# Kernel tuning notes

Measured on AMD Instinct MI355X. Metric: run time of the kernel, lower is better.

## Reference

```python
import jax, jax.numpy as jnp
import numpy as np

IGNORE_INDEX = -100
BETA = 0.1

B, T, H, V = 4, 512, 1024, 32000  # sequences, tokens/seq, hidden, vocab


def setup_inputs() -> dict:
    key = jax.random.key(0)
    ks = jax.random.split(key, 9)
    scale = 1.0 / np.sqrt(H)
    return {
        "_input": jax.random.normal(ks[0], (B * T, H), jnp.float32),
        "weight": jax.random.normal(ks[1], (V, H), jnp.float32) * scale,
        "target": jax.random.randint(ks[2], (B * T,), 0, V, jnp.int64),
        "bias": jax.random.normal(ks[3], (V,), jnp.float32) * 0.01,
        "preference_labels": jax.random.bernoulli(ks[4], 0.5, (B,)),
        "ref_input": jax.random.normal(ks[5], (B * T, H), jnp.float32),
        "ref_weight": jax.random.normal(ks[6], (V, H), jnp.float32) * scale,
        "ref_bias": jax.random.normal(ks[7], (V,), jnp.float32) * 0.01,
        "kl": jax.random.uniform(ks[8], (1,), jnp.float32),
    }


def _seq_log_prob(x, w, b, target):
    # x: (B*T, H), w: (V, H), b: (V,) -> per-sequence summed target logprob (B,)
    logits = x @ w.T + b  # (B*T, V) -- the tensor the fused kernel avoids
    logp = jax.nn.log_softmax(logits, axis=-1)
    safe_tgt = jnp.clip(target, 0, logp.shape[-1] - 1)
    tok_logp = jnp.take_along_axis(logp, safe_tgt[:, None], axis=-1)[:, 0]
    mask = target != IGNORE_INDEX
    tok_logp = jnp.where(mask, tok_logp, 0.0).reshape(B, T)
    return tok_logp.sum(axis=-1)  # average_log_prob=False


def reference(_input, weight, target, bias, preference_labels, ref_input, ref_weight, ref_bias, kl):
    pol_logp = _seq_log_prob(_input, weight, bias, target)          # (B,)
    ref_logp = _seq_log_prob(ref_input, ref_weight, ref_bias, target)  # (B,)
    logratios = pol_logp - ref_logp
    multiplier = jnp.where(preference_labels, 1.0, -1.0)
    losses = 1.0 - jax.nn.sigmoid(BETA * (logratios - kl[0]) * multiplier)
    loss = losses.sum() / target.shape[0]  # divide by full_target.shape[0] = B*T
    rewards = BETA * logratios
    chosen_rewards_sum = (rewards * preference_labels).sum()
    rejected_rewards_sum = (rewards * (~preference_labels)).sum()
    return loss, chosen_rewards_sum, rejected_rewards_sum
```

## Files before the change

kernel.cpp:

```cpp
#include <hip/hip_runtime.h>

#define BT    2048
#define HDIM  1024
#define VDIM  32000
#define NSEQ  4
#define BETA  0.1f
#define IGNORE_IDX (-100)

typedef __attribute__((ext_vector_type(8))) short bf16x8;
typedef __attribute__((ext_vector_type(8))) unsigned short u16x8;
typedef __attribute__((ext_vector_type(4))) float f32x4;

#define WS_BF_BYTE  32768
#define XBF_OFF     0
#define XRBF_OFF    (BT * HDIM)
#define WBF_OFF     (2 * BT * HDIM)
#define WRBF_OFF    (2 * BT * HDIM + VDIM * HDIM)
#define CVT_TOTAL   (2 * BT * HDIM + 2 * VDIM * HDIM)
#define WS_NEED     ((size_t)WS_BF_BYTE + (size_t)CVT_TOTAL * 2)

__device__ __forceinline__ unsigned short f2bf_rne(float f) {
  unsigned int u = __builtin_bit_cast(unsigned int, f);
  u += 0x7fffu + ((u >> 16) & 1u);
  return (unsigned short)(u >> 16);
}

__device__ __forceinline__ u16x8 cvt8(float4 a, float4 b) {
  u16x8 v;
  v[0] = f2bf_rne(a.x); v[1] = f2bf_rne(a.y); v[2] = f2bf_rne(a.z); v[3] = f2bf_rne(a.w);
  v[4] = f2bf_rne(b.x); v[5] = f2bf_rne(b.y); v[6] = f2bf_rne(b.z); v[7] = f2bf_rne(b.w);
  return v;
}

__global__ __launch_bounds__(256) void kto_zero_ws(float* p) {
  p[blockIdx.x * 256 + threadIdx.x] = 0.0f;
}

__global__ __launch_bounds__(256) void kto_convert(
    const float* __restrict__ X, const float* __restrict__ Xr,
    const float* __restrict__ W, const float* __restrict__ Wr,
    unsigned short* __restrict__ bf)
{
  size_t gid8 = ((size_t)blockIdx.x * 256 + threadIdx.x) * 8;
  if (gid8 >= (size_t)CVT_TOTAL) return;
  const float* src; size_t off;
  if (gid8 < (size_t)XRBF_OFF)      { src = X;  off = gid8; }
  else if (gid8 < (size_t)WBF_OFF)  { src = Xr; off = gid8 - XRBF_OFF; }
  else if (gid8 < (size_t)WRBF_OFF) { src = W;  off = gid8 - WBF_OFF; }
  else                              { src = Wr; off = gid8 - WRBF_OFF; }
  const float4* p = (const float4*)(src + off);
  float4 a = p[0], b = p[1];
  *(u16x8*)(bf + gid8) = cvt8(a, b);
}

#define GLD16(g, l) __builtin_amdgcn_global_load_lds( \
    (const __attribute__((address_space(1))) unsigned int*)(g), \
    (__attribute__((address_space(3))) unsigned int*)(l), 16, 0, 0)

__global__ __launch_bounds__(256) void kto_lse_gemm_fast(
    const unsigned short* __restrict__ bf,
    const float* __restrict__ Bp, const float* __restrict__ Br,
    const int* __restrict__ target,
    float* __restrict__ ws_se, float* __restrict__ ws_tg)
{
  const int model = blockIdx.z;
  const unsigned short* __restrict__ Xb = bf + (model ? XRBF_OFF : XBF_OFF);
  const unsigned short* __restrict__ Wb = bf + (model ? WRBF_OFF : WBF_OFF);
  const float* __restrict__ Bv = model ? Br : Bp;

  __shared__ unsigned short Asm[128 * 32];
  __shared__ unsigned short Bsm[128 * 32];

  const int tid  = threadIdx.x;
  const int wave = tid >> 6;
  const int lane = tid & 63;
  const int q    = lane >> 4;
  const int c    = lane & 15;
  const int mW   = (wave >> 1) * 64;
  const int nW   = (wave & 1) * 64;
  const int mBase = blockIdx.x * 128;
  const int nBase = blockIdx.y * 128;

  const int lrow = lane >> 2;
  const int lchk = (lane & 3) ^ ((lane >> 3) & 3);

  const char* gsrc[4];
  unsigned short* ldst[4];
  #pragma unroll
  for (int j = 0; j < 4; ++j) {
    const int seg = wave * 4 + j;
    if (seg < 8) {
      const int row = mBase + seg * 16 + lrow;
      gsrc[j] = (const char*)Xb + (size_t)row * (HDIM * 2) + lchk * 16;
      ldst[j] = &Asm[seg * 512];
    } else {
      const int row = nBase + (seg - 8) * 16 + lrow;
      gsrc[j] = (const char*)Wb + (size_t)row * (HDIM * 2) + lchk * 16;
      ldst[j] = &Bsm[(seg - 8) * 512];
    }
  }

  const int swz = (q ^ ((c >> 1) & 3)) * 8;

  f32x4 acc[4][4] = {};

  for (int kt = 0; kt < HDIM / 32; ++kt) {
    __syncthreads();
    const size_t kb = (size_t)kt * 64;
    #pragma unroll
    for (int j = 0; j < 4; ++j)
      GLD16(gsrc[j] + kb, ldst[j]);
    __syncthreads();

    bf16x8 afr[4], bfr[4];
    #pragma unroll
    for (int mi = 0; mi < 4; ++mi)
      afr[mi] = *(const bf16x8*)&Asm[(mW + mi * 16 + c) * 32 + swz];
    #pragma unroll
    for (int ni = 0; ni < 4; ++ni)
      bfr[ni] = *(const bf16x8*)&Bsm[(nW + ni * 16 + c) * 32 + swz];
    #pragma unroll
    for (int mi = 0; mi < 4; ++mi)
      #pragma unroll
      for (int ni = 0; ni < 4; ++ni)
        acc[mi][ni] = __builtin_amdgcn_mfma_f32_16x16x32_bf16(afr[mi], bfr[ni], acc[mi][ni], 0, 0, 0);
  }

  float se_acc[4][4] = {};
  float tg_acc[4][4] = {};
  int tgt_idx[4][4];
  #pragma unroll
  for (int mi = 0; mi < 4; ++mi)
    #pragma unroll
    for (int r = 0; r < 4; ++r)
      tgt_idx[mi][r] = target[mBase + mW + mi * 16 + q * 4 + r];

  #pragma unroll
  for (int ni = 0; ni < 4; ++ni) {
    const int col = nBase + nW + ni * 16 + c;
    const float bv = Bv[col];
    #pragma unroll
    for (int mi = 0; mi < 4; ++mi)
      #pragma unroll
      for (int r = 0; r < 4; ++r) {
        float logit = acc[mi][ni][r] + bv;
        se_acc[mi][r] += __expf(logit);
        if (tgt_idx[mi][r] == col) tg_acc[mi][r] += logit;
      }
  }

  #pragma unroll
  for (int mi = 0; mi < 4; ++mi)
    #pragma unroll
    for (int r = 0; r < 4; ++r) {
      float s = se_acc[mi][r];
      float t = tg_acc[mi][r];
      #pragma unroll
      for (int off = 1; off < 16; off <<= 1) {
        s += __shfl_xor(s, off, 64);
        t += __shfl_xor(t, off, 64);
      }
      if (c == ((mi << 2) | r)) {
        const int row = mBase + mW + mi * 16 + q * 4 + r;
        atomicAdd(&ws_se[model * BT + row], s);
        atomicAdd(&ws_tg[model * BT + row], t);
      }
    }
}

#define SBM 128
#define SBN 128
#define SBK 32
#define SVSLICE 1280
#define SNITER  (SVSLICE / SBN)
#define SKTILES (HDIM / SBK)
#define SLDK    (SBK + 8)

__device__ __forceinline__ void cvt_store8s(unsigned short* dst, float4 a, float4 b) {
  *(u16x8*)dst = cvt8(a, b);
}

__global__ __launch_bounds__(256) void kto_lse_gemm_slow(
    const float* __restrict__ Xp, const float* __restrict__ Wp, const float* __restrict__ Bp,
    const float* __restrict__ Xr, const float* __restrict__ Wr, const float* __restrict__ Br,
    const int* __restrict__ target, float* __restrict__ ws_se, float* __restrict__ ws_tg)
{
  const int model = blockIdx.z;
  const float* __restrict__ X  = model ? Xr : Xp;
  const float* __restrict__ W  = model ? Wr : Wp;
  const float* __restrict__ Bv = model ? Br : Bp;

  __shared__ unsigned short Asm[SBM][SLDK];
  __shared__ unsigned short Bsm[SBN][SLDK];

  const int tid  = threadIdx.x;
  const int wave = tid >> 6;
  const int lane = tid & 63;
  const int q    = lane >> 4;
  const int c    = lane & 15;
  const int mW   = (wave >> 1) * 64;
  const int nW   = (wave & 1) * 64;
  const int mBase = blockIdx.x * SBM;
  const int vBase = blockIdx.y * SVSLICE;

  const int srow = tid >> 1;
  const int scol = (tid & 1) << 4;

  int tgt_idx[4][4];
  #pragma unroll
  for (int mi = 0; mi < 4; ++mi)
    #pragma unroll
    for (int r = 0; r < 4; ++r)
      tgt_idx[mi][r] = target[mBase + mW + mi * 16 + q * 4 + r];

  float se_acc[4][4] = {};
  float tg_acc[4][4] = {};

  for (int it = 0; it < SNITER; ++it) {
    const int nIterBase = vBase + it * SBN;
    f32x4 acc[4][4] = {};

    for (int kt = 0; kt < SKTILES; ++kt) {
      __syncthreads();
      {
        const float4* a4 = (const float4*)(X + (size_t)(mBase + srow) * HDIM + kt * SBK + scol);
        float4 a0 = a4[0], a1 = a4[1], a2 = a4[2], a3 = a4[3];
        const float4* b4 = (const float4*)(W + (size_t)(nIterBase + srow) * HDIM + kt * SBK + scol);
        float4 b0 = b4[0], b1 = b4[1], b2 = b4[2], b3 = b4[3];
        cvt_store8s(&Asm[srow][scol],     a0, a1);
        cvt_store8s(&Asm[srow][scol + 8], a2, a3);
        cvt_store8s(&Bsm[srow][scol],     b0, b1);
        cvt_store8s(&Bsm[srow][scol + 8], b2, b3);
      }
      __syncthreads();

      bf16x8 afr[4], bfr[4];
      #pragma unroll
      for (int mi = 0; mi < 4; ++mi)
        afr[mi] = *(const bf16x8*)&Asm[mW + mi * 16 + c][q * 8];
      #pragma unroll
      for (int ni = 0; ni < 4; ++ni)
        bfr[ni] = *(const bf16x8*)&Bsm[nW + ni * 16 + c][q * 8];
      #pragma unroll
      for (int mi = 0; mi < 4; ++mi)
        #pragma unroll
        for (int ni = 0; ni < 4; ++ni)
          acc[mi][ni] = __builtin_amdgcn_mfma_f32_16x16x32_bf16(afr[mi], bfr[ni], acc[mi][ni], 0, 0, 0);
    }

    #pragma unroll
    for (int ni = 0; ni < 4; ++ni) {
      const int col = nIterBase + nW + ni * 16 + c;
      const float bv = Bv[col];
      #pragma unroll
      for (int mi = 0; mi < 4; ++mi)
        #pragma unroll
        for (int r = 0; r < 4; ++r) {
          float logit = acc[mi][ni][r] + bv;
          se_acc[mi][r] += __expf(logit);
          if (tgt_idx[mi][r] == col) tg_acc[mi][r] += logit;
        }
    }
  }

  #pragma unroll
  for (int mi = 0; mi < 4; ++mi)
    #pragma unroll
    for (int r = 0; r < 4; ++r) {
      float s = se_acc[mi][r];
      float t = tg_acc[mi][r];
      #pragma unroll
      for (int off = 1; off < 16; off <<= 1) {
        s += __shfl_xor(s, off, 64);
        t += __shfl_xor(t, off, 64);
      }
      if (c == 0) {
        const int row = mBase + mW + mi * 16 + q * 4 + r;
        atomicAdd(&ws_se[model * BT + row], s);
        atomicAdd(&ws_tg[model * BT + row], t);
      }
    }
}

__global__ __launch_bounds__(256) void kto_finalize(
    const float* __restrict__ ws_se, const float* __restrict__ ws_tg,
    const int* __restrict__ target, const int* __restrict__ pref,
    const float* __restrict__ kl, float* __restrict__ out)
{
  __shared__ float lr[NSEQ];
  const int tid = threadIdx.x;
  if (tid < NSEQ) lr[tid] = 0.0f;
  __syncthreads();
  for (int t = tid; t < BT; t += 256) {
    float d = 0.0f;
    if (target[t] != IGNORE_IDX) {
      float lp_p = ws_tg[t]      - __logf(ws_se[t]);
      float lp_r = ws_tg[BT + t] - __logf(ws_se[BT + t]);
      d = lp_p - lp_r;
    }
    atomicAdd(&lr[t >> 9], d);
  }
  __syncthreads();
  if (tid == 0) {
    float loss = 0.f, ch = 0.f, rj = 0.f;
    const float klv = kl[0];
    for (int b = 0; b < NSEQ; ++b) {
      float logratio = lr[b];
      bool p = pref[b] != 0;
      float mult = p ? 1.0f : -1.0f;
      float z = BETA * (logratio - klv) * mult;
      float sig = 1.0f / (1.0f + __expf(-z));
      loss += 1.0f - sig;
      float rw = BETA * logratio;
      if (p) ch += rw; else rj += rw;
    }
    out[0] = loss / (float)BT;
    out[1] = ch;
    out[2] = rj;
  }
}

extern "C" void kernel_launch(void* const* d_in, const int* in_sizes, int n_in,
                              void* d_out, int out_size, void* d_ws, size_t ws_size,
                              hipStream_t stream) {
  (void)in_sizes; (void)n_in; (void)out_size;
  const float* X    = (const float*)d_in[0];
  const float* W    = (const float*)d_in[1];
  const int*   tgt  = (const int*)d_in[2];
  const float* bias = (const float*)d_in[3];
  const int*   pref = (const int*)d_in[4];
  const float* Xr   = (const float*)d_in[5];
  const float* Wr   = (const float*)d_in[6];
  const float* br   = (const float*)d_in[7];
  const float* kl   = (const float*)d_in[8];
  float* out = (float*)d_out;

  float* ws_se = (float*)d_ws;
  float* ws_tg = ws_se + 2 * BT;

  kto_zero_ws<<<32, 256, 0, stream>>>(ws_se);

  if (ws_size >= WS_NEED) {
    unsigned short* bf = (unsigned short*)((char*)d_ws + WS_BF_BYTE);
    kto_convert<<<(CVT_TOTAL / 2048), 256, 0, stream>>>(X, Xr, W, Wr, bf);
    dim3 grid(BT / 128, VDIM / 128, 2);
    kto_lse_gemm_fast<<<grid, 256, 0, stream>>>(bf, bias, br, tgt, ws_se, ws_tg);
  } else {
    dim3 grid(BT / SBM, VDIM / SVSLICE, 2);
    kto_lse_gemm_slow<<<grid, 256, 0, stream>>>(X, W, bias, Xr, Wr, br, tgt, ws_se, ws_tg);
  }

  kto_finalize<<<1, 256, 0, stream>>>(ws_se, ws_tg, tgt, pref, kl, out);
}
```

Measured before the change: 671.1 us.

## Use 256x256 tiles with 4-stage LDS pipeline and grid remap in fused GEMM

Reworks the bf16 MFMA logsumexp GEMM to 256x256 tiles with 512 threads. Global-to-LDS loads now run through a 4-slot ring two k-steps ahead and are split across two half-steps separated by barriers, using s_setprio around the MFMA bursts. Workgroups are remapped so neighbouring blocks share row tiles for better L2 reuse. The aim is to hide memory latency and raise arithmetic intensity, at the cost of 128KB LDS per block, more registers for 8x4 accumulators, and fragile hand-placed waitcnt/barrier ordering.

```diff
diff --git a/kernel.cpp b/kernel.cpp
--- a/kernel.cpp
+++ b/kernel.cpp
@@ -57,7 +57,7 @@
     (const __attribute__((address_space(1))) unsigned int*)(g), \
     (__attribute__((address_space(3))) unsigned int*)(l), 16, 0, 0)
 
-__global__ __launch_bounds__(256) void kto_lse_gemm_fast(
+__global__ __launch_bounds__(512, 2) void kto_lse_gemm_fast(
     const unsigned short* __restrict__ bf,
     const float* __restrict__ Bp, const float* __restrict__ Br,
     const int* __restrict__ target,
@@ -68,104 +68,140 @@
   const unsigned short* __restrict__ Wb = bf + (model ? WRBF_OFF : WBF_OFF);
   const float* __restrict__ Bv = model ? Br : Bp;
 
-  __shared__ unsigned short Asm[128 * 32];
-  __shared__ unsigned short Bsm[128 * 32];
+  const int lin  = blockIdx.x + (blockIdx.y << 3);
+  const int wgid = (lin & 7) * 125 + (lin >> 3);
+  const int mBase = (wgid & 7) * 256;
+  const int nBase = (wgid >> 3) * 256;
+
+  __shared__ unsigned short lds[4 * 16384];
 
   const int tid  = threadIdx.x;
   const int wave = tid >> 6;
   const int lane = tid & 63;
   const int q    = lane >> 4;
   const int c    = lane & 15;
-  const int mW   = (wave >> 1) * 64;
-  const int nW   = (wave & 1) * 64;
-  const int mBase = blockIdx.x * 128;
-  const int nBase = blockIdx.y * 128;
+  const int wm   = wave >> 2;
+  const int wn   = wave & 3;
 
   const int lrow = lane >> 2;
   const int lchk = (lane & 3) ^ ((lane >> 3) & 3);
 
   const char* gsrc[4];
-  unsigned short* ldst[4];
+  int ldst[4];
   #pragma unroll
   for (int j = 0; j < 4; ++j) {
     const int seg = wave * 4 + j;
-    if (seg < 8) {
+    if (seg < 16) {
       const int row = mBase + seg * 16 + lrow;
       gsrc[j] = (const char*)Xb + (size_t)row * (HDIM * 2) + lchk * 16;
-      ldst[j] = &Asm[seg * 512];
+      ldst[j] = seg * 512;
     } else {
-      const int row = nBase + (seg - 8) * 16 + lrow;
+      const int row = nBase + (seg - 16) * 16 + lrow;
       gsrc[j] = (const char*)Wb + (size_t)row * (HDIM * 2) + lchk * 16;
-      ldst[j] = &Bsm[(seg - 8) * 512];
-    }
-  }
-
-  const int swz = (q ^ ((c >> 1) & 3)) * 8;
-
-  f32x4 acc[4][4] = {};
-
-  for (int kt = 0; kt < HDIM / 32; ++kt) {
-    __syncthreads();
-    const size_t kb = (size_t)kt * 64;
+      ldst[j] = 8192 + (seg - 16) * 512;
+    }
+  }
+
+  #pragma unroll
+  for (int u = 0; u < 2; ++u) {
+    unsigned short* dst = &lds[u * 16384];
     #pragma unroll
     for (int j = 0; j < 4; ++j)
-      GLD16(gsrc[j] + kb, ldst[j]);
-    __syncthreads();
+      GLD16(gsrc[j] + u * 64, &dst[ldst[j]]);
+  }
+  asm volatile("s_waitcnt vmcnt(4)" ::: "memory");
+  __builtin_amdgcn_s_barrier();
+
+  const int swz   = (q ^ ((c >> 1) & 3)) * 8;
+  const int aBase = (wm * 128 + c) * 32 + swz;
+  const int bBase = 8192 + (wn * 64 + c) * 32 + swz;
+
+  f32x4 acc[8][4] = {};
+
+  for (int u = 0; u < 32; ++u) {
+    const unsigned short* sl = &lds[(u & 3) * 16384];
+    unsigned short* dst = &lds[((u + 2) & 3) * 16384];
+    const int kb2 = ((u + 2) & 31) * 64;
 
     bf16x8 afr[4], bfr[4];
     #pragma unroll
+    for (int ni = 0; ni < 4; ++ni)
+      bfr[ni] = *(const bf16x8*)&sl[bBase + ni * 512];
+    #pragma unroll
     for (int mi = 0; mi < 4; ++mi)
-      afr[mi] = *(const bf16x8*)&Asm[(mW + mi * 16 + c) * 32 + swz];
-    #pragma unroll
-    for (int ni = 0; ni < 4; ++ni)
-      bfr[ni] = *(const bf16x8*)&Bsm[(nW + ni * 16 + c) * 32 + swz];
+      afr[mi] = *(const bf16x8*)&sl[aBase + mi * 512];
+    GLD16(gsrc[0] + kb2, &dst[ldst[0]]);
+    GLD16(gsrc[1] + kb2, &dst[ldst[1]]);
+    __builtin_amdgcn_s_barrier();
+    asm volatile("s_waitcnt lgkmcnt(0)" ::: "memory");
+    __builtin_amdgcn_sched_barrier(0);
+    __builtin_amdgcn_s_setprio(1);
     #pragma unroll
     for (int mi = 0; mi < 4; ++mi)
       #pragma unroll
       for (int ni = 0; ni < 4; ++ni)
         acc[mi][ni] = __builtin_amdgcn_mfma_f32_16x16x32_bf16(afr[mi], bfr[ni], acc[mi][ni], 0, 0, 0);
-  }
-
-  float se_acc[4][4] = {};
-  float tg_acc[4][4] = {};
-  int tgt_idx[4][4];
-  #pragma unroll
-  for (int mi = 0; mi < 4; ++mi)
-    #pragma unroll
-    for (int r = 0; r < 4; ++r)
-      tgt_idx[mi][r] = target[mBase + mW + mi * 16 + q * 4 + r];
-
+    __builtin_amdgcn_s_setprio(0);
+    __builtin_amdgcn_s_barrier();
+
+    #pragma unroll
+    for (int mi = 0; mi < 4; ++mi)
+      afr[mi] = *(const bf16x8*)&sl[aBase + 2048 + mi * 512];
+    GLD16(gsrc[2] + kb2, &dst[ldst[2]]);
+    GLD16(gsrc[3] + kb2, &dst[ldst[3]]);
+    asm volatile("s_waitcnt vmcnt(4)" ::: "memory");
+    __builtin_amdgcn_s_barrier();
+    asm volatile("s_waitcnt lgkmcnt(0)" ::: "memory");
+    __builtin_amdgcn_sched_barrier(0);
+    __builtin_amdgcn_s_setprio(1);
+    #pragma unroll
+    for (int mi = 0; mi < 4; ++mi)
+      #pragma unroll
+      for (int ni = 0; ni < 4; ++ni)
+        acc[mi + 4][ni] = __builtin_amdgcn_mfma_f32_16x16x32_bf16(afr[mi], bfr[ni], acc[mi + 4][ni], 0, 0, 0);
+    __builtin_amdgcn_s_setprio(0);
+    __builtin_amdgcn_s_barrier();
+  }
+
+  float bv[4]; int colc[4];
   #pragma unroll
   for (int ni = 0; ni < 4; ++ni) {
-    const int col = nBase + nW + ni * 16 + c;
-    const float bv = Bv[col];
-    #pragma unroll
-    for (int mi = 0; mi < 4; ++mi)
+    colc[ni] = nBase + wn * 64 + ni * 16 + c;
+    bv[ni] = Bv[colc[ni]];
+  }
+
+  #pragma unroll
+  for (int mi = 0; mi < 8; ++mi) {
+    const int rowb = mBase + wm * 128 + mi * 16 + q * 4;
+    int tgt4[4];
+    #pragma unroll
+    for (int r = 0; r < 4; ++r) tgt4[r] = target[rowb + r];
+    float se[4] = {0.f, 0.f, 0.f, 0.f};
+    float tg[4] = {0.f, 0.f, 0.f, 0.f};
+    #pragma unroll
+    for (int ni = 0; ni < 4; ++ni)
       #pragma unroll
       for (int r = 0; r < 4; ++r) {
-        float logit = acc[mi][ni][r] + bv;
-        se_acc[mi][r] += __expf(logit);
-        if (tgt_idx[mi][r] == col) tg_acc[mi][r] += logit;
-      }
-  }
-
-  #pragma unroll
-  for (int mi = 0; mi < 4; ++mi)
+        float logit = acc[mi][ni][r] + bv[ni];
+        se[r] += __expf(logit);
+        if (tgt4[r] == colc[ni]) tg[r] += logit;
+      }
     #pragma unroll
     for (int r = 0; r < 4; ++r) {
-      float s = se_acc[mi][r];
-      float t = tg_acc[mi][r];
+      float s = se[r];
+      float t = tg[r];
       #pragma unroll
       for (int off = 1; off < 16; off <<= 1) {
         s += __shfl_xor(s, off, 64);
         t += __shfl_xor(t, off, 64);
       }
-      if (c == ((mi << 2) | r)) {
-        const int row = mBase + mW + mi * 16 + q * 4 + r;
+      if (c == ((mi * 4 + r) & 15)) {
+        const int row = rowb + r;
         atomicAdd(&ws_se[model * BT + row], s);
         atomicAdd(&ws_tg[model * BT + row], t);
       }
     }
+  }
 }
 
 #define SBM 128
@@ -343,8 +379,8 @@
   if (ws_size >= WS_NEED) {
     unsigned short* bf = (unsigned short*)((char*)d_ws + WS_BF_BYTE);
     kto_convert<<<(CVT_TOTAL / 2048), 256, 0, stream>>>(X, Xr, W, Wr, bf);
-    dim3 grid(BT / 128, VDIM / 128, 2);
-    kto_lse_gemm_fast<<<grid, 256, 0, stream>>>(bf, bias, br, tgt, ws_se, ws_tg);
+    dim3 grid(BT / 256, VDIM / 256, 2);
+    kto_lse_gemm_fast<<<grid, 512, 0, stream>>>(bf, bias, br, tgt, ws_se, ws_tg);
   } else {
     dim3 grid(BT / SBM, VDIM / SVSLICE, 2);
     kto_lse_gemm_slow<<<grid, 256, 0, stream>>>(X, W, bias, Xr, Wr, br, tgt, ws_se, ws_tg);
```

Measured after the change: 615.0 us. 8.4% less time.

## Triple-buffer LDS K-loop with async prefetch and remap workgroups for L2 locality

Applied to the files above, without the earlier changes.

Replaces the single-buffered, two-barrier K loop with a three-stage LDS ring. Global-to-LDS loads are issued two iterations ahead and the loop uses one barrier per step, with a manual vmcnt wait, so memory latency overlaps the MFMA work. It also remaps the linear block id so consecutive workgroups share weight tiles, and it sets launch bounds to target three blocks per CU. The trade-off is more LDS per block (48KB) and a manual waitcnt/barrier scheme that is fragile: the last iterations issue redundant wrapped loads.

```diff
diff --git a/kernel.cpp b/kernel.cpp
--- a/kernel.cpp
+++ b/kernel.cpp
@@ -57,7 +57,7 @@
     (const __attribute__((address_space(1))) unsigned int*)(g), \
     (__attribute__((address_space(3))) unsigned int*)(l), 16, 0, 0)
 
-__global__ __launch_bounds__(256) void kto_lse_gemm_fast(
+__global__ __launch_bounds__(256, 3) void kto_lse_gemm_fast(
     const unsigned short* __restrict__ bf,
     const float* __restrict__ Bp, const float* __restrict__ Br,
     const int* __restrict__ target,
@@ -68,8 +68,12 @@
   const unsigned short* __restrict__ Wb = bf + (model ? WRBF_OFF : WBF_OFF);
   const float* __restrict__ Bv = model ? Br : Bp;
 
-  __shared__ unsigned short Asm[128 * 32];
-  __shared__ unsigned short Bsm[128 * 32];
+  const int lin  = blockIdx.x + (blockIdx.y << 4);
+  const int wgid = (lin & 7) * 500 + (lin >> 3);
+  const int mBase = (wgid & 15) * 128;
+  const int nBase = (wgid >> 4) * 128;
+
+  __shared__ unsigned short lds[3 * 8192];
 
   const int tid  = threadIdx.x;
   const int wave = tid >> 6;
@@ -78,52 +82,71 @@
   const int c    = lane & 15;
   const int mW   = (wave >> 1) * 64;
   const int nW   = (wave & 1) * 64;
-  const int mBase = blockIdx.x * 128;
-  const int nBase = blockIdx.y * 128;
 
   const int lrow = lane >> 2;
   const int lchk = (lane & 3) ^ ((lane >> 3) & 3);
 
   const char* gsrc[4];
-  unsigned short* ldst[4];
+  int ldst[4];
   #pragma unroll
   for (int j = 0; j < 4; ++j) {
     const int seg = wave * 4 + j;
     if (seg < 8) {
       const int row = mBase + seg * 16 + lrow;
       gsrc[j] = (const char*)Xb + (size_t)row * (HDIM * 2) + lchk * 16;
-      ldst[j] = &Asm[seg * 512];
+      ldst[j] = seg * 512;
     } else {
       const int row = nBase + (seg - 8) * 16 + lrow;
       gsrc[j] = (const char*)Wb + (size_t)row * (HDIM * 2) + lchk * 16;
-      ldst[j] = &Bsm[(seg - 8) * 512];
+      ldst[j] = 4096 + (seg - 8) * 512;
     }
   }
 
   const int swz = (q ^ ((c >> 1) & 3)) * 8;
 
+  #pragma unroll
+  for (int uu = 0; uu < 2; ++uu) {
+    unsigned short* dst = &lds[uu * 8192];
+    #pragma unroll
+    for (int j = 0; j < 4; ++j)
+      GLD16(gsrc[j] + uu * 64, &dst[ldst[j]]);
+  }
+  asm volatile("s_waitcnt vmcnt(4)" ::: "memory");
+  __builtin_amdgcn_s_barrier();
+  __builtin_amdgcn_sched_barrier(0);
+
   f32x4 acc[4][4] = {};
-
-  for (int kt = 0; kt < HDIM / 32; ++kt) {
-    __syncthreads();
-    const size_t kb = (size_t)kt * 64;
-    #pragma unroll
-    for (int j = 0; j < 4; ++j)
-      GLD16(gsrc[j] + kb, ldst[j]);
-    __syncthreads();
-
+  int cur = 0;
+
+  for (int u = 0; u < 32; ++u) {
+    const unsigned short* sl = &lds[cur * 8192];
     bf16x8 afr[4], bfr[4];
     #pragma unroll
+    for (int ni = 0; ni < 4; ++ni)
+      bfr[ni] = *(const bf16x8*)&sl[4096 + (nW + ni * 16 + c) * 32 + swz];
+    #pragma unroll
     for (int mi = 0; mi < 4; ++mi)
-      afr[mi] = *(const bf16x8*)&Asm[(mW + mi * 16 + c) * 32 + swz];
-    #pragma unroll
-    for (int ni = 0; ni < 4; ++ni)
-      bfr[ni] = *(const bf16x8*)&Bsm[(nW + ni * 16 + c) * 32 + swz];
+      afr[mi] = *(const bf16x8*)&sl[(mW + mi * 16 + c) * 32 + swz];
+
+    int nx2 = cur + 2; if (nx2 >= 3) nx2 -= 3;
+    unsigned short* dst = &lds[nx2 * 8192];
+    const size_t kb = (size_t)((u + 2) & 31) * 64;
+    GLD16(gsrc[0] + kb, &dst[ldst[0]]);
+    GLD16(gsrc[1] + kb, &dst[ldst[1]]);
+    GLD16(gsrc[2] + kb, &dst[ldst[2]]);
+    GLD16(gsrc[3] + kb, &dst[ldst[3]]);
+
     #pragma unroll
     for (int mi = 0; mi < 4; ++mi)
       #pragma unroll
       for (int ni = 0; ni < 4; ++ni)
         acc[mi][ni] = __builtin_amdgcn_mfma_f32_16x16x32_bf16(afr[mi], bfr[ni], acc[mi][ni], 0, 0, 0);
+
+    asm volatile("s_waitcnt vmcnt(4)" ::: "memory");
+    __builtin_amdgcn_s_barrier();
+    __builtin_amdgcn_sched_barrier(0);
+
+    cur = (cur == 2) ? 0 : cur + 1;
   }
 
   float se_acc[4][4] = {};
```

New measurement: 649.1 us. 1.03x faster.
